# Kernel tuning notes

Measured on AMD Instinct MI355X. Metric: run time of the kernel, lower is better.

Reference implementation:

```python
import jax, jax.numpy as jnp
import numpy as np

DT = 0.1  # fixed dt offset from init_kwargs


def setup_inputs() -> dict:
    key = jax.random.key(0)
    ks = jax.random.split(key, 8)
    B_, L, D, N = 4, 4096, 128, 16
    s = 1.0 / np.sqrt(D)
    # S4D-Real init: A_n = -(n+1), repeated over input_dim (random_init=False)
    A = jnp.broadcast_to(-(jnp.arange(N, dtype=jnp.float32) + 1.0), (D, N))
    return {
        "x": jax.random.normal(ks[0], (B_, L, D), dtype=jnp.float32),
        "A": A,
        "Wb": jax.random.uniform(ks[1], (N, D), minval=-s, maxval=s, dtype=jnp.float32),
        "bb": jax.random.uniform(ks[2], (N,), minval=-s, maxval=s, dtype=jnp.float32),
        "Wc": jax.random.uniform(ks[3], (N, D), minval=-s, maxval=s, dtype=jnp.float32),
        "bc": jax.random.uniform(ks[4], (N,), minval=-s, maxval=s, dtype=jnp.float32),
        "Wd": jax.random.uniform(ks[5], (1, D), minval=-s, maxval=s, dtype=jnp.float32),
        "bd": jax.random.uniform(ks[6], (1,), minval=-s, maxval=s, dtype=jnp.float32),
    }


def reference(x, A, Wb, bb, Wc, bc, Wd, bd):
    # x: [B, L, D]; A: [D, N]
    Bp = x @ Wb.T + bb                                   # [B, L, N]  (self.sb)
    C = x @ Wc.T + bc                                    # [B, L, N]  (self.sc)
    # DeltaNetwork: softplus(Linear(x)) + dt, repeated over input_dim
    delta = jax.nn.softplus(x @ Wd.T + bd) + DT          # [B, L, 1]
    delta = jnp.broadcast_to(delta, x.shape)             # [B, L, D]
    # discretize: A_bar = exp(dt*A); B_bar = (1 - exp(-dt*A)) * (dt x B)
    dA = delta[..., None] * A                            # [B, L, D, N]
    A_bar = jnp.exp(dA)
    Bx = (1.0 - jnp.exp(-dA)) * delta[..., None] * Bp[:, :, None, :] * x[..., None]  # B_bar * x_t

    def step(h, inp):
        A_t, Bx_t, C_t = inp                             # [B,D,N],[B,D,N],[B,N]
        h = A_t * h + Bx_t
        y_t = jnp.sum(h * C_t[:, None, :], axis=-1)      # [B, D]
        return h, y_t

    h0 = jnp.zeros((x.shape[0], x.shape[2], A.shape[1]), x.dtype)
    _, y = jax.lax.scan(
        step, h0,
        (A_bar.transpose(1, 0, 2, 3), Bx.transpose(1, 0, 2, 3), C.transpose(1, 0, 2)),
    )
    return y.transpose(1, 0, 2)                          # [B, L, D]
```

## Files before the change

### kernel.cpp

```cpp
#include <hip/hip_runtime.h>
#include <math.h>

#define B_ 4
#define L_ 4096
#define D_ 128
#define N_ 16
#define DT_ 0.1f
#define CHUNK_ 32
#define NC_ 128

#define WT_OFF   0
#define ABAR_OFF 4608
#define COEF_OFF (ABAR_OFF + 262144)
#define CC_OFF   (COEF_OFF + 262144)
#define HL_OFF   (CC_OFF + 262144)
#define H0_OFF   (HL_OFF + 1048576)
#define P_OFF    (H0_OFF + 1048576)

__global__ __launch_bounds__(256) void k0_transpose(const float* __restrict__ Wb,
                                                    const float* __restrict__ Wc,
                                                    const float* __restrict__ Wd,
                                                    float* __restrict__ ws) {
    float* Wt = ws + WT_OFF;
    int t = threadIdx.x;
    for (int i = t; i < 128 * 33; i += 256) {
        int k = i / 33, c = i % 33;
        float v;
        if (c < 16)      v = Wb[c * 128 + k];
        else if (c < 32) v = Wc[(c - 16) * 128 + k];
        else             v = Wd[k];
        Wt[k * 36 + c] = v;
    }
}

__global__ __launch_bounds__(256) void k1_proj(const float* __restrict__ x,
                                               const float* __restrict__ A,
                                               const float* __restrict__ bb,
                                               const float* __restrict__ bc,
                                               const float* __restrict__ bd,
                                               float* __restrict__ ws) {
    __shared__ float xs[64][129];
    __shared__ float part[4][33][64];

    const float* Wt = ws + WT_OFF;
    float* abar_o = ws + ABAR_OFF;
    float* coef_o = ws + COEF_OFF;
    float* cc_o   = ws + CC_OFF;

    const int t = threadIdx.x;
    const size_t row0 = (size_t)blockIdx.x * 64;

    const float4* xg = (const float4*)(x + row0 * 128);
    for (int i = t; i < 2048; i += 256) {
        float4 v = xg[i];
        int r = i >> 5;
        int c0 = (i & 31) << 2;
        xs[r][c0]     = v.x;
        xs[r][c0 + 1] = v.y;
        xs[r][c0 + 2] = v.z;
        xs[r][c0 + 3] = v.w;
    }
    __syncthreads();

    const int w = __builtin_amdgcn_readfirstlane(t >> 6);
    const int lane = t & 63;

    float acc[33];
#pragma unroll
    for (int c = 0; c < 33; ++c) acc[c] = 0.f;

    const float* wbase = Wt + (size_t)w * 32 * 36;
#pragma unroll 4
    for (int kk = 0; kk < 32; ++kk) {
        float xv = xs[lane][w * 32 + kk];
        const float* wk = wbase + kk * 36;
#pragma unroll
        for (int c = 0; c < 33; ++c) acc[c] = fmaf(xv, wk[c], acc[c]);
    }

#pragma unroll
    for (int c = 0; c < 33; ++c) part[w][c][lane] = acc[c];
    __syncthreads();

    const int r = t & 63;
    const int g = t >> 6;
    float dsum = part[0][32][r] + part[1][32][r] + part[2][32][r] + part[3][32][r];
    float zd = dsum + bd[0];
    float sp = fmaxf(zd, 0.f) + log1pf(expf(-fabsf(zd)));
    float delta = sp + DT_;

    size_t orow = (row0 + (size_t)r) * 16;
#pragma unroll
    for (int j = 0; j < 4; ++j) {
        int n = g * 4 + j;
        float Bp = part[0][n][r] + part[1][n][r] + part[2][n][r] + part[3][n][r] + bb[n];
        float Cv = part[0][16 + n][r] + part[1][16 + n][r] + part[2][16 + n][r] + part[3][16 + n][r] + bc[n];
        float An = A[n];
        float dA = delta * An;
        float ab = expf(dA);
        float em = expf(-dA);
        float cf = (1.f - em) * delta * Bp;
        abar_o[orow + n] = ab;
        coef_o[orow + n] = cf;
        cc_o[orow + n]   = Cv;
    }
}

__global__ __launch_bounds__(256) void k2a_chunk(const float* __restrict__ x,
                                                 float* __restrict__ ws) {
    const float* abar = ws + ABAR_OFF;
    const float* coef = ws + COEF_OFF;
    float* hL = ws + HL_OFF;
    float* Pp = ws + P_OFF;

    const int gw = blockIdx.x * 4 + (threadIdx.x >> 6);
    const int lane = threadIdx.x & 63;
    const int b = gw >> 10;
    const int dgrp = (gw >> 7) & 7;
    const int c = gw & 127;
    const int ng = lane >> 4;
    const int dq = lane & 15;
    const int d = dgrp * 16 + dq;
    const int l0 = c * CHUNK_;
    const size_t sbase = ((size_t)b * L_ + l0) * 16 + ng * 4;
    const float* px = x + ((size_t)b * L_ + l0) * 128 + d;

    float h0v = 0.f, h1v = 0.f, h2v = 0.f, h3v = 0.f;
    float P0 = 1.f, P1 = 1.f, P2 = 1.f, P3 = 1.f;
#pragma unroll 4
    for (int t = 0; t < CHUNK_; ++t) {
        float4 a4 = *(const float4*)(abar + sbase + t * 16);
        float4 c4 = *(const float4*)(coef + sbase + t * 16);
        float xv = px[t * 128];
        h0v = fmaf(a4.x, h0v, c4.x * xv);
        h1v = fmaf(a4.y, h1v, c4.y * xv);
        h2v = fmaf(a4.z, h2v, c4.z * xv);
        h3v = fmaf(a4.w, h3v, c4.w * xv);
        P0 *= a4.x; P1 *= a4.y; P2 *= a4.z; P3 *= a4.w;
    }
    float4 hv = make_float4(h0v, h1v, h2v, h3v);
    *(float4*)(hL + (((size_t)(b * NC_ + c)) * 128 + d) * 16 + ng * 4) = hv;
    if (dq == 0) {
        float4 pv = make_float4(P0, P1, P2, P3);
        *(float4*)(Pp + ((size_t)(b * NC_ + c)) * 16 + ng * 4) = pv;
    }
}

__global__ __launch_bounds__(256) void k2b_combine(float* __restrict__ ws) {
    const float* hL = ws + HL_OFF;
    const float* Pp = ws + P_OFF;
    float* h0 = ws + H0_OFF;
    const int tid = blockIdx.x * 256 + threadIdx.x;
    const int b = tid >> 11;
    const int dn = tid & 2047;
    const int n = tid & 15;

    float h = 0.f;
    h0[((size_t)(b * NC_)) * 2048 + dn] = 0.f;
    for (int c = 1; c < NC_; ++c) {
        float hl = hL[((size_t)(b * NC_ + c - 1)) * 2048 + dn];
        float p  = Pp[((size_t)(b * NC_ + c - 1)) * 16 + n];
        h = fmaf(p, h, hl);
        h0[((size_t)(b * NC_ + c)) * 2048 + dn] = h;
    }
}

__global__ __launch_bounds__(256) void k2c_scan(const float* __restrict__ x,
                                                const float* __restrict__ ws,
                                                float* __restrict__ y) {
    const float* abar = ws + ABAR_OFF;
    const float* coef = ws + COEF_OFF;
    const float* cc   = ws + CC_OFF;
    const float* h0   = ws + H0_OFF;

    const int gw = blockIdx.x * 4 + (threadIdx.x >> 6);
    const int lane = threadIdx.x & 63;
    const int b = gw >> 10;
    const int dgrp = (gw >> 7) & 7;
    const int c = gw & 127;
    const int ng = lane >> 4;
    const int dq = lane & 15;
    const int d = dgrp * 16 + dq;
    const int l0 = c * CHUNK_;
    const size_t sbase = ((size_t)b * L_ + l0) * 16 + ng * 4;
    const float* px = x + ((size_t)b * L_ + l0) * 128 + d;
    float* py = y + ((size_t)b * L_ + l0) * 128 + d;

    float4 h4 = *(const float4*)(h0 + (((size_t)(b * NC_ + c)) * 128 + d) * 16 + ng * 4);
    float h0v = h4.x, h1v = h4.y, h2v = h4.z, h3v = h4.w;

#pragma unroll 4
    for (int t = 0; t < CHUNK_; ++t) {
        float4 a4 = *(const float4*)(abar + sbase + t * 16);
        float4 c4 = *(const float4*)(coef + sbase + t * 16);
        float4 C4 = *(const float4*)(cc   + sbase + t * 16);
        float xv = px[t * 128];
        h0v = fmaf(a4.x, h0v, c4.x * xv);
        h1v = fmaf(a4.y, h1v, c4.y * xv);
        h2v = fmaf(a4.z, h2v, c4.z * xv);
        h3v = fmaf(a4.w, h3v, c4.w * xv);
        float yv = h0v * C4.x + h1v * C4.y + h2v * C4.z + h3v * C4.w;
        yv += __shfl_xor(yv, 16);
        yv += __shfl_xor(yv, 32);
        if (ng == 0) py[t * 128] = yv;
    }
}

extern "C" void kernel_launch(void* const* d_in, const int* in_sizes, int n_in,
                              void* d_out, int out_size, void* d_ws, size_t ws_size,
                              hipStream_t stream) {
    const float* x  = (const float*)d_in[0];
    const float* A  = (const float*)d_in[1];
    const float* Wb = (const float*)d_in[2];
    const float* bb = (const float*)d_in[3];
    const float* Wc = (const float*)d_in[4];
    const float* bc = (const float*)d_in[5];
    const float* Wd = (const float*)d_in[6];
    const float* bd = (const float*)d_in[7];
    float* ws = (float*)d_ws;
    float* y  = (float*)d_out;

    k0_transpose<<<1, 256, 0, stream>>>(Wb, Wc, Wd, ws);
    k1_proj<<<256, 256, 0, stream>>>(x, A, bb, bc, bd, ws);
    k2a_chunk<<<1024, 256, 0, stream>>>(x, ws);
    k2b_combine<<<32, 256, 0, stream>>>(ws);
    k2c_scan<<<1024, 256, 0, stream>>>(x, ws, y);
}
```

Measured before the change: 149.6 us.

## Drop transpose and combine kernels; fold chunk-prefix combine into scan kernel

Removes the weight-transpose kernel and has the projection kernel read Wb/Wc/Wd directly, splitting each row tile across two blocks (B-side and C-side) with a smaller shared buffer. The serial cross-chunk combine kernel is eliminated; each scan wave now recomputes its starting state by folding all preceding chunk summaries itself. This saves two launches and a serial low-parallelism pass, but adds redundant, imbalanced work (up to 127 combine steps for late chunks) and extra reads of hL in the scan kernel.

```diff
diff --git a/kernel.cpp b/kernel.cpp
--- a/kernel.cpp
+++ b/kernel.cpp
@@ -9,46 +9,31 @@
 #define CHUNK_ 32
 #define NC_ 128
 
-#define WT_OFF   0
-#define ABAR_OFF 4608
+#define ABAR_OFF 0
 #define COEF_OFF (ABAR_OFF + 262144)
 #define CC_OFF   (COEF_OFF + 262144)
 #define HL_OFF   (CC_OFF + 262144)
-#define H0_OFF   (HL_OFF + 1048576)
-#define P_OFF    (H0_OFF + 1048576)
-
-__global__ __launch_bounds__(256) void k0_transpose(const float* __restrict__ Wb,
-                                                    const float* __restrict__ Wc,
-                                                    const float* __restrict__ Wd,
-                                                    float* __restrict__ ws) {
-    float* Wt = ws + WT_OFF;
-    int t = threadIdx.x;
-    for (int i = t; i < 128 * 33; i += 256) {
-        int k = i / 33, c = i % 33;
-        float v;
-        if (c < 16)      v = Wb[c * 128 + k];
-        else if (c < 32) v = Wc[(c - 16) * 128 + k];
-        else             v = Wd[k];
-        Wt[k * 36 + c] = v;
-    }
-}
+#define P_OFF    (HL_OFF + 1048576)
 
 __global__ __launch_bounds__(256) void k1_proj(const float* __restrict__ x,
                                                const float* __restrict__ A,
+                                               const float* __restrict__ Wb,
                                                const float* __restrict__ bb,
+                                               const float* __restrict__ Wc,
                                                const float* __restrict__ bc,
+                                               const float* __restrict__ Wd,
                                                const float* __restrict__ bd,
                                                float* __restrict__ ws) {
     __shared__ float xs[64][129];
-    __shared__ float part[4][33][64];
-
-    const float* Wt = ws + WT_OFF;
+    __shared__ float proj[64][18];
+
     float* abar_o = ws + ABAR_OFF;
     float* coef_o = ws + COEF_OFF;
     float* cc_o   = ws + CC_OFF;
 
     const int t = threadIdx.x;
-    const size_t row0 = (size_t)blockIdx.x * 64;
+    const int bt = blockIdx.x & 1;
+    const size_t row0 = (size_t)(blockIdx.x >> 1) * 64;
 
     const float4* xg = (const float4*)(x + row0 * 128);
     for (int i = t; i < 2048; i += 256) {
@@ -65,44 +50,71 @@
     const int w = __builtin_amdgcn_readfirstlane(t >> 6);
     const int lane = t & 63;
 
-    float acc[33];
-#pragma unroll
-    for (int c = 0; c < 33; ++c) acc[c] = 0.f;
-
-    const float* wbase = Wt + (size_t)w * 32 * 36;
-#pragma unroll 4
-    for (int kk = 0; kk < 32; ++kk) {
-        float xv = xs[lane][w * 32 + kk];
-        const float* wk = wbase + kk * 36;
-#pragma unroll
-        for (int c = 0; c < 33; ++c) acc[c] = fmaf(xv, wk[c], acc[c]);
-    }
-
-#pragma unroll
-    for (int c = 0; c < 33; ++c) part[w][c][lane] = acc[c];
+    const float* cbase = (bt == 0 ? Wb : Wc) + (size_t)w * 4 * 128;
+    float a0 = 0.f, a1 = 0.f, a2 = 0.f, a3 = 0.f;
+#pragma unroll 8
+    for (int k = 0; k < 128; ++k) {
+        float xv = xs[lane][k];
+        a0 = fmaf(xv, cbase[k],       a0);
+        a1 = fmaf(xv, cbase[128 + k], a1);
+        a2 = fmaf(xv, cbase[256 + k], a2);
+        a3 = fmaf(xv, cbase[384 + k], a3);
+    }
+    proj[lane][w * 4]     = a0;
+    proj[lane][w * 4 + 1] = a1;
+    proj[lane][w * 4 + 2] = a2;
+    proj[lane][w * 4 + 3] = a3;
+    if (bt == 0 && w == 3) {
+        float ad = 0.f;
+#pragma unroll 8
+        for (int k = 0; k < 128; ++k) ad = fmaf(xs[lane][k], Wd[k], ad);
+        proj[lane][16] = ad;
+    }
     __syncthreads();
 
     const int r = t & 63;
     const int g = t >> 6;
-    float dsum = part[0][32][r] + part[1][32][r] + part[2][32][r] + part[3][32][r];
-    float zd = dsum + bd[0];
-    float sp = fmaxf(zd, 0.f) + log1pf(expf(-fabsf(zd)));
-    float delta = sp + DT_;
-
-    size_t orow = (row0 + (size_t)r) * 16;
-#pragma unroll
-    for (int j = 0; j < 4; ++j) {
-        int n = g * 4 + j;
-        float Bp = part[0][n][r] + part[1][n][r] + part[2][n][r] + part[3][n][r] + bb[n];
-        float Cv = part[0][16 + n][r] + part[1][16 + n][r] + part[2][16 + n][r] + part[3][16 + n][r] + bc[n];
-        float An = A[n];
-        float dA = delta * An;
-        float ab = expf(dA);
-        float em = expf(-dA);
-        float cf = (1.f - em) * delta * Bp;
-        abar_o[orow + n] = ab;
-        coef_o[orow + n] = cf;
-        cc_o[orow + n]   = Cv;
+    const int n0 = g * 4;
+    const size_t orow = (row0 + (size_t)r) * 16 + n0;
+
+    if (bt == 0) {
+        float zd = proj[r][16] + bd[0];
+        float sp = fmaxf(zd, 0.f) + log1pf(expf(-fabsf(zd)));
+        float delta = sp + DT_;
+        float4 ab4, cf4;
+        {
+            float Bp = proj[r][n0] + bb[n0];
+            float dA = delta * A[n0];
+            ab4.x = expf(dA);
+            cf4.x = (1.f - expf(-dA)) * delta * Bp;
+        }
+        {
+            float Bp = proj[r][n0 + 1] + bb[n0 + 1];
+            float dA = delta * A[n0 + 1];
+            ab4.y = expf(dA);
+            cf4.y = (1.f - expf(-dA)) * delta * Bp;
+        }
+        {
+            float Bp = proj[r][n0 + 2] + bb[n0 + 2];
+            float dA = delta * A[n0 + 2];
+            ab4.z = expf(dA);
+            cf4.z = (1.f - expf(-dA)) * delta * Bp;
+        }
+        {
+            float Bp = proj[r][n0 + 3] + bb[n0 + 3];
+            float dA = delta * A[n0 + 3];
+            ab4.w = expf(dA);
+            cf4.w = (1.f - expf(-dA)) * delta * Bp;
+        }
+        *(float4*)(abar_o + orow) = ab4;
+        *(float4*)(coef_o + orow) = cf4;
+    } else {
+        float4 cv4;
+        cv4.x = proj[r][n0]     + bc[n0];
+        cv4.y = proj[r][n0 + 1] + bc[n0 + 1];
+        cv4.z = proj[r][n0 + 2] + bc[n0 + 2];
+        cv4.w = proj[r][n0 + 3] + bc[n0 + 3];
+        *(float4*)(cc_o + orow) = cv4;
     }
 }
 
@@ -127,7 +139,7 @@
 
     float h0v = 0.f, h1v = 0.f, h2v = 0.f, h3v = 0.f;
     float P0 = 1.f, P1 = 1.f, P2 = 1.f, P3 = 1.f;
-#pragma unroll 4
+#pragma unroll 8
     for (int t = 0; t < CHUNK_; ++t) {
         float4 a4 = *(const float4*)(abar + sbase + t * 16);
         float4 c4 = *(const float4*)(coef + sbase + t * 16);
@@ -138,30 +150,11 @@
         h3v = fmaf(a4.w, h3v, c4.w * xv);
         P0 *= a4.x; P1 *= a4.y; P2 *= a4.z; P3 *= a4.w;
     }
-    float4 hv = make_float4(h0v, h1v, h2v, h3v);
-    *(float4*)(hL + (((size_t)(b * NC_ + c)) * 128 + d) * 16 + ng * 4) = hv;
+    *(float4*)(hL + (((size_t)(b * NC_ + c)) * 128 + d) * 16 + ng * 4) =
+        make_float4(h0v, h1v, h2v, h3v);
     if (dq == 0) {
-        float4 pv = make_float4(P0, P1, P2, P3);
-        *(float4*)(Pp + ((size_t)(b * NC_ + c)) * 16 + ng * 4) = pv;
-    }
-}
-
-__global__ __launch_bounds__(256) void k2b_combine(float* __restrict__ ws) {
-    const float* hL = ws + HL_OFF;
-    const float* Pp = ws + P_OFF;
-    float* h0 = ws + H0_OFF;
-    const int tid = blockIdx.x * 256 + threadIdx.x;
-    const int b = tid >> 11;
-    const int dn = tid & 2047;
-    const int n = tid & 15;
-
-    float h = 0.f;
-    h0[((size_t)(b * NC_)) * 2048 + dn] = 0.f;
-    for (int c = 1; c < NC_; ++c) {
-        float hl = hL[((size_t)(b * NC_ + c - 1)) * 2048 + dn];
-        float p  = Pp[((size_t)(b * NC_ + c - 1)) * 16 + n];
-        h = fmaf(p, h, hl);
-        h0[((size_t)(b * NC_ + c)) * 2048 + dn] = h;
+        *(float4*)(Pp + ((size_t)(b * NC_ + c)) * 16 + ng * 4) =
+            make_float4(P0, P1, P2, P3);
     }
 }
 
@@ -171,7 +164,8 @@
     const float* abar = ws + ABAR_OFF;
     const float* coef = ws + COEF_OFF;
     const float* cc   = ws + CC_OFF;
-    const float* h0   = ws + H0_OFF;
+    const float* hL   = ws + HL_OFF;
+    const float* Pp   = ws + P_OFF;
 
     const int gw = blockIdx.x * 4 + (threadIdx.x >> 6);
     const int lane = threadIdx.x & 63;
@@ -186,8 +180,18 @@
     const float* px = x + ((size_t)b * L_ + l0) * 128 + d;
     float* py = y + ((size_t)b * L_ + l0) * 128 + d;
 
-    float4 h4 = *(const float4*)(h0 + (((size_t)(b * NC_ + c)) * 128 + d) * 16 + ng * 4);
-    float h0v = h4.x, h1v = h4.y, h2v = h4.z, h3v = h4.w;
+    float h0v = 0.f, h1v = 0.f, h2v = 0.f, h3v = 0.f;
+    const float* hLp = hL + ((size_t)b * NC_) * 2048 + d * 16 + ng * 4;
+    const float* Pq  = Pp + ((size_t)b * NC_) * 16 + ng * 4;
+#pragma unroll 4
+    for (int cc2 = 0; cc2 < c; ++cc2) {
+        float4 hl4 = *(const float4*)(hLp + (size_t)cc2 * 2048);
+        float4 p4  = *(const float4*)(Pq + (size_t)cc2 * 16);
+        h0v = fmaf(p4.x, h0v, hl4.x);
+        h1v = fmaf(p4.y, h1v, hl4.y);
+        h2v = fmaf(p4.z, h2v, hl4.z);
+        h3v = fmaf(p4.w, h3v, hl4.w);
+    }
 
 #pragma unroll 4
     for (int t = 0; t < CHUNK_; ++t) {
@@ -220,9 +224,7 @@
     float* ws = (float*)d_ws;
     float* y  = (float*)d_out;
 
-    k0_transpose<<<1, 256, 0, stream>>>(Wb, Wc, Wd, ws);
-    k1_proj<<<256, 256, 0, stream>>>(x, A, bb, bc, bd, ws);
+    k1_proj<<<512, 256, 0, stream>>>(x, A, Wb, bb, Wc, bc, Wd, bd, ws);
     k2a_chunk<<<1024, 256, 0, stream>>>(x, ws);
-    k2b_combine<<<32, 256, 0, stream>>>(ws);
     k2c_scan<<<1024, 256, 0, stream>>>(x, ws, y);
 }
```

Result: slower. 155.9 us (+4.2%).
